# Optimization experiments

Measured on AMD Instinct MI355X. Metric: run time of the kernel, lower is better.

Reference implementation:

```python
import jax, jax.numpy as jnp
import numpy as np

EPS = 1e-06


def setup_inputs() -> dict:
    key = jax.random.key(0)
    k1, k2, k3 = jax.random.split(key, 3)
    B, H, S, D = 4, 16, 4096, 64
    query = jax.random.normal(k1, (B, H, S, D), dtype=jnp.float32)
    key_t = jax.random.normal(k2, (B, H, S, D), dtype=jnp.float32)
    value = jax.random.normal(k3, (B, H, S, D), dtype=jnp.float32)
    return {"query": query, "key": key_t, "value": value}


def _cosformer_features(x, cos_idx, sin_idx):
    # x: [B,H,S,D]; cos_idx/sin_idx: [S,1] -> features [B,H,S,2D]
    x_relu = jax.nn.relu(x)
    return jnp.concatenate([x_relu * cos_idx, x_relu * sin_idx], axis=-1)


def reference(query, key, value):
    B, H, S, D = query.shape
    query = query / jnp.sqrt(jnp.asarray(D, dtype=query.dtype))
    # idx = (pi/2) * [1..S]; angles divided by seq_len
    ang = (jnp.pi / 2) * jnp.arange(1, S + 1, dtype=query.dtype) / S  # [S]
    cos_idx = jnp.cos(ang)[:, None]  # [S,1]
    sin_idx = jnp.sin(ang)[:, None]  # [S,1]
    q_cs = _cosformer_features(query, cos_idx, sin_idx)  # [B,H,S,2D]
    k_cs = _cosformer_features(key, cos_idx, sin_idx)    # [B,H,S,2D]
    # norm: 1 / clamp(q_cs . sum_l(k_cs), eps)
    k_sum = jnp.sum(k_cs, axis=-2)  # [B,H,2D]
    norm = 1.0 / jnp.maximum(jnp.einsum('bhld,bhd->bhl', q_cs, k_sum), EPS)  # [B,H,S]
    # linear attention: KV aggregation then query projection
    kv = jnp.einsum('bhld,bhlm->bhdm', k_cs, value)  # [B,H,2D,D]
    out = jnp.einsum('bhld,bhdm->bhlm', q_cs, kv) * norm[..., None]  # [B,H,S,D]
    return out
```

## Files before the change

kernel.cpp:

```cpp
#include <hip/hip_runtime.h>
#include <hip/hip_bf16.h>
#include <math.h>
#include <stdint.h>

#define BHN    64
#define SEQ    4096
#define DIM    64
#define NCHUNK 8
#define CHUNK  (SEQ / NCHUNK)
#define KSTEP  32
#define NIT    (CHUNK / KSTEP)
#define KVF    (128 * DIM)
#define STRIDE_C ((size_t)BHN * KVF + (size_t)BHN * 128)
#define KSBASE ((size_t)BHN * KVF)
#define FRAGH  10240
#define LPADT  40

typedef __bf16 bf16x8v __attribute__((ext_vector_type(8)));
typedef float  f32x4v  __attribute__((ext_vector_type(4)));

__device__ inline f32x4v mfma16(bf16x8v a, bf16x8v b, f32x4v c) {
    return __builtin_amdgcn_mfma_f32_16x16x32_bf16(a, b, c, 0, 0, 0);
}

__device__ inline unsigned pk2(float a, float b) {
    __hip_bfloat162 t(__float2bfloat16(a), __float2bfloat16(b));
    return *(unsigned*)&t;
}

__device__ __forceinline__ void barrier_noflush() {
    asm volatile("s_waitcnt lgkmcnt(0)" ::: "memory");
    __builtin_amdgcn_s_barrier();
    asm volatile("" ::: "memory");
}

__device__ __forceinline__ void gload16(const float* g, const float* lds_base) {
    __builtin_amdgcn_global_load_lds(
        (const __attribute__((address_space(1))) void*)(uintptr_t)g,
        (__attribute__((address_space(3)))  void*)(uintptr_t)lds_base,
        16, 0, 0);
}

template<int USE_ATOMIC>
__global__ __launch_bounds__(512) void cosformer_kv_mfma(
    const float* __restrict__ K, const float* __restrict__ V,
    float* __restrict__ part)
{
    __shared__ float  rawK[3][KSTEP][DIM];
    __shared__ float  rawV[3][KSTEP][DIM];
    __shared__ ushort ktc[DIM][LPADT];
    __shared__ ushort kts[DIM][LPADT];
    __shared__ ushort vtt[DIM][LPADT];

    const int bh    = blockIdx.x / NCHUNK;
    const int chunk = blockIdx.x % NCHUNK;
    const int row0  = chunk * CHUNK;
    const float* Kb = K + (size_t)bh * SEQ * DIM;
    const float* Vb = V + (size_t)bh * SEQ * DIM;

    const int tid  = threadIdx.x;
    const int lane = tid & 63;
    const int w    = tid >> 6;
    const int g2    = (tid >> 4) & 15;
    const int dq    = (tid & 15) * 4;
    const int kvsel = tid >> 8;
    const int frow = lane & 15;
    const int kgrp = lane >> 4;
    const int d0   = (w & 3) * 16 + frow;

    f32x4v acc[5];
    #pragma unroll
    for (int t = 0; t < 5; ++t) acc[t] = (f32x4v){0.f, 0.f, 0.f, 0.f};

    bf16x8v onef;
    #pragma unroll
    for (int j = 0; j < 8; ++j) onef[j] = (frow == 0) ? (__bf16)1.0f : (__bf16)0.0f;

    auto STAGE = [&](int it) {
        const int buf = it % 3;
        const size_t go = (size_t)(row0 + it * KSTEP) * DIM + w * 256 + lane * 4;
        gload16(Kb + go, &rawK[buf][w * 4][0]);
        gload16(Vb + go, &rawV[buf][w * 4][0]);
    };

    auto TRANSFORM = [&](int it) {
        const int buf = it % 3;
        const int r = 2 * g2;
        if (kvsel == 0) {
            float4 k0 = *(const float4*)&rawK[buf][r][dq];
            float4 k1 = *(const float4*)&rawK[buf][r + 1][dq];
            const int l0 = row0 + it * KSTEP + r;
            const float CC = 1.5707963267948966f / (float)SEQ;
            float s0v, c0, s1v, c1;
            __sincosf(CC * (float)(l0 + 1), &s0v, &c0);
            __sincosf(CC * (float)(l0 + 2), &s1v, &c1);
            float a0[4] = {k0.x, k0.y, k0.z, k0.w};
            float a1[4] = {k1.x, k1.y, k1.z, k1.w};
            #pragma unroll
            for (int i = 0; i < 4; ++i) {
                const int d = dq + i;
                const int c = g2 ^ (4 * ((d >> 2) & 3));
                float r0 = fmaxf(a0[i], 0.f), r1 = fmaxf(a1[i], 0.f);
                ((unsigned*)&ktc[d][0])[c] = pk2(r0 * c0,  r1 * c1);
                ((unsigned*)&kts[d][0])[c] = pk2(r0 * s0v, r1 * s1v);
            }
        } else {
            float4 v0q = *(const float4*)&rawV[buf][r][dq];
            float4 v1q = *(const float4*)&rawV[buf][r + 1][dq];
            float a0[4] = {v0q.x, v0q.y, v0q.z, v0q.w};
            float a1[4] = {v1q.x, v1q.y, v1q.z, v1q.w};
            #pragma unroll
            for (int i = 0; i < 4; ++i) {
                const int d = dq + i;
                const int c = g2 ^ (4 * ((d >> 2) & 3));
                ((unsigned*)&vtt[d][0])[c] = pk2(a0[i], a1[i]);
            }
        }
    };

    STAGE(0);
    STAGE(1);

    #pragma unroll 1
    for (int it = 0; it < NIT; ++it) {
        if (it + 1 < NIT) asm volatile("s_waitcnt vmcnt(2)" ::: "memory");
        else              asm volatile("s_waitcnt vmcnt(0)" ::: "memory");
        __builtin_amdgcn_sched_barrier(0);
        barrier_noflush();

        if (it + 2 < NIT) STAGE(it + 2);

        TRANSFORM(it);
        barrier_noflush();

        const ushort (*ap)[LPADT] = (w < 4) ? ktc : kts;
        {
            const int ca = (kgrp * 4) ^ (4 * ((d0 >> 2) & 3));
            bf16x8v a = *(const bf16x8v*)&ap[d0][2 * ca];
            #pragma unroll
            for (int nt = 0; nt < 4; ++nt) {
                const int dn = nt * 16 + frow;
                const int cb = (kgrp * 4) ^ (4 * ((dn >> 2) & 3));
                bf16x8v b = *(const bf16x8v*)&vtt[dn][2 * cb];
                acc[nt] = mfma16(a, b, acc[nt]);
            }
            acc[4] = mfma16(a, onef, acc[4]);
        }
    }

    const int fb = w * 16 + kgrp * 4;
    if (USE_ATOMIC) {
        float* pb = part + (size_t)bh * KVF;
        float* ps = part + KSBASE + bh * 128;
        #pragma unroll
        for (int nt = 0; nt < 4; ++nt)
            #pragma unroll
            for (int r = 0; r < 4; ++r)
                atomicAdd(&pb[(size_t)(fb + r) * DIM + nt * 16 + frow], acc[nt][r]);
        if (frow == 0)
            #pragma unroll
            for (int r = 0; r < 4; ++r) atomicAdd(&ps[fb + r], acc[4][r]);
    } else {
        float* pb = part + STRIDE_C * chunk + (size_t)bh * KVF;
        float* ps = part + STRIDE_C * chunk + KSBASE + bh * 128;
        #pragma unroll
        for (int nt = 0; nt < 4; ++nt)
            #pragma unroll
            for (int r = 0; r < 4; ++r)
                pb[(size_t)(fb + r) * DIM + nt * 16 + frow] = acc[nt][r];
        if (frow == 0)
            #pragma unroll
            for (int r = 0; r < 4; ++r) ps[fb + r] = acc[4][r];
    }
}

template<int NC>
__global__ __launch_bounds__(256) void reduce_pack(
    const float* __restrict__ part, __hip_bfloat16* __restrict__ bfrag)
{
    size_t o = (size_t)blockIdx.x * 256 + threadIdx.x;
    float s = 0.f;
    #pragma unroll
    for (int c = 0; c < NC; ++c) s += part[(size_t)c * STRIDE_C + o];
    if (o < KSBASE) {
        int head = (int)(o >> 13);
        int r = (int)(o & 8191);
        int k = r >> 6, n = r & 63;
        int t = n >> 4, ks = k >> 5, lg = (k >> 3) & 3, j = k & 7;
        int lane = lg * 16 + (n & 15);
        bfrag[(size_t)head * FRAGH + (size_t)(((t * 4 + ks) * 64 + lane) * 8 + j)] =
            __float2bfloat16(s);
    } else {
        int r = (int)(o - KSBASE);
        int head = r >> 7, k = r & 127;
        int ks = k >> 5, lg = (k >> 3) & 3, j = k & 7;
        bfrag[(size_t)head * FRAGH + (size_t)(((16 + ks) * 64 + lg * 16) * 8 + j)] =
            __float2bfloat16(s);
    }
}

__global__ __launch_bounds__(256) void cosformer_out_mfma(
    const float* __restrict__ Q, const __hip_bfloat16* __restrict__ bfrag,
    float* __restrict__ out)
{
    __shared__ __hip_bfloat16 sb[FRAGH];
    const int head = blockIdx.x >> 3;
    const int tile = blockIdx.x & 7;
    const int tid  = threadIdx.x;

    {
        const float4* src = (const float4*)(bfrag + (size_t)head * FRAGH);
        float4* dst = (float4*)sb;
        #pragma unroll
        for (int i = 0; i < 5; ++i) dst[tid + 256 * i] = src[tid + 256 * i];
    }

    const int lane = tid & 63;
    const int w    = tid >> 6;
    const int mrow = lane & 15;
    const int kgrp = lane >> 4;

    const float* Qb = Q + (size_t)head * SEQ * DIM;
    float*       Ob = out + (size_t)head * SEQ * DIM;
    const int rowblk = tile * 512;

    float4 qb[2][4];
    #pragma unroll
    for (int m = 0; m < 2; ++m) {
        const float4* qr = (const float4*)(Qb + (size_t)(rowblk + w * 32 + m * 16 + mrow) * DIM);
        qb[m][0] = qr[kgrp * 2];
        qb[m][1] = qr[kgrp * 2 + 1];
        qb[m][2] = qr[8 + kgrp * 2];
        qb[m][3] = qr[8 + kgrp * 2 + 1];
    }

    barrier_noflush();

    #pragma unroll
    for (int g = 0; g < 4; ++g) {
        const int base = rowblk + (g * 4 + w) * 32;

        bf16x8v af[2][4];
        #pragma unroll
        for (int m = 0; m < 2; ++m) {
            int arow = base + m * 16 + mrow;
            float ang = 1.5707963267948966f * (float)(arow + 1) / (float)SEQ;
            float sn, cn;
            __sincosf(ang, &sn, &cn);
            float crs = cn * 0.125f, srs = sn * 0.125f;
            float lo[8] = {qb[m][0].x, qb[m][0].y, qb[m][0].z, qb[m][0].w,
                           qb[m][1].x, qb[m][1].y, qb[m][1].z, qb[m][1].w};
            float hi[8] = {qb[m][2].x, qb[m][2].y, qb[m][2].z, qb[m][2].w,
                           qb[m][3].x, qb[m][3].y, qb[m][3].z, qb[m][3].w};
            #pragma unroll
            for (int j = 0; j < 8; ++j) {
                float rl = fmaxf(lo[j], 0.f);
                float rh = fmaxf(hi[j], 0.f);
                af[m][0][j] = (__bf16)(rl * crs);
                af[m][1][j] = (__bf16)(rh * crs);
                af[m][2][j] = (__bf16)(rl * srs);
                af[m][3][j] = (__bf16)(rh * srs);
            }
        }

        if (g < 3) {
            #pragma unroll
            for (int m = 0; m < 2; ++m) {
                const float4* qr = (const float4*)(Qb + (size_t)(rowblk + ((g + 1) * 4 + w) * 32 + m * 16 + mrow) * DIM);
                qb[m][0] = qr[kgrp * 2];
                qb[m][1] = qr[kgrp * 2 + 1];
                qb[m][2] = qr[8 + kgrp * 2];
                qb[m][3] = qr[8 + kgrp * 2 + 1];
            }
        }

        f32x4v acc[2][5];
        #pragma unroll
        for (int m = 0; m < 2; ++m)
            #pragma unroll
            for (int t = 0; t < 5; ++t)
                acc[m][t] = (f32x4v){0.f, 0.f, 0.f, 0.f};

        #pragma unroll
        for (int t = 0; t < 5; ++t)
            #pragma unroll
            for (int ks = 0; ks < 4; ++ks) {
                bf16x8v bf = *(const bf16x8v*)&sb[(size_t)(((t * 4 + ks) * 64 + lane) * 8)];
                acc[0][t] = mfma16(af[0][ks], bf, acc[0][t]);
                acc[1][t] = mfma16(af[1][ks], bf, acc[1][t]);
            }

        #pragma unroll
        for (int m = 0; m < 2; ++m) {
            #pragma unroll
            for (int r = 0; r < 4; ++r) {
                float den = __shfl(acc[m][4][r], lane & 48, 64);
                float invd = 1.0f / fmaxf(den, 1e-6f);
                int row = base + m * 16 + kgrp * 4 + r;
                float* op = Ob + (size_t)row * DIM + mrow;
                op[0]  = acc[m][0][r] * invd;
                op[16] = acc[m][1][r] * invd;
                op[32] = acc[m][2][r] * invd;
                op[48] = acc[m][3][r] * invd;
            }
        }
    }
}

extern "C" void kernel_launch(void* const* d_in, const int* in_sizes, int n_in,
                              void* d_out, int out_size, void* d_ws, size_t ws_size,
                              hipStream_t stream) {
    const float* Q = (const float*)d_in[0];
    const float* K = (const float*)d_in[1];
    const float* V = (const float*)d_in[2];
    float* out = (float*)d_out;
    float* ws  = (float*)d_ws;

    const size_t frag_bytes = (size_t)FRAGH * BHN * sizeof(__hip_bfloat16);
    const size_t need_full  = (size_t)NCHUNK * STRIDE_C * sizeof(float) + frag_bytes;

    if (ws_size >= need_full) {
        float* part = ws;
        __hip_bfloat16* bfrag = (__hip_bfloat16*)(ws + (size_t)NCHUNK * STRIDE_C);
        hipMemsetAsync(bfrag, 0, frag_bytes, stream);
        hipLaunchKernelGGL((cosformer_kv_mfma<0>), dim3(BHN * NCHUNK), dim3(512), 0, stream,
                           K, V, part);
        hipLaunchKernelGGL((reduce_pack<NCHUNK>), dim3((int)(STRIDE_C / 256)), dim3(256), 0, stream,
                           part, bfrag);
        hipLaunchKernelGGL(cosformer_out_mfma, dim3(BHN * 8), dim3(256), 0, stream,
                           Q, bfrag, out);
    } else {
        float* part = ws;
        __hip_bfloat16* bfrag = (__hip_bfloat16*)(ws + STRIDE_C);
        hipMemsetAsync(part, 0, STRIDE_C * sizeof(float), stream);
        hipMemsetAsync(bfrag, 0, frag_bytes, stream);
        hipLaunchKernelGGL((cosformer_kv_mfma<1>), dim3(BHN * NCHUNK), dim3(512), 0, stream,
                           K, V, part);
        hipLaunchKernelGGL((reduce_pack<1>), dim3((int)(STRIDE_C / 256)), dim3(256), 0, stream,
                           part, bfrag);
        hipLaunchKernelGGL(cosformer_out_mfma, dim3(BHN * 8), dim3(256), 0, stream,
                           Q, bfrag, out);
    }
}
```

Before: 71.63 us.

## Issue all chunk loads upfront and double the sequence chunk count

Doubles the number of sequence chunks per batch-head, so each block covers 256 rows (8 iterations). The 3-buffer rolling prefetch is replaced by issuing every K/V load for the whole chunk at kernel start into LDS, with per-iteration vmcnt waits that count down. This aims to keep more memory requests in flight and give the GPU twice as many blocks. In exchange, LDS use grows to about 128KB per block, which may limit blocks per CU, and the partial-sum reduction or atomic traffic doubles.

```diff
diff --git a/kernel.cpp b/kernel.cpp
--- a/kernel.cpp
+++ b/kernel.cpp
@@ -6,7 +6,7 @@
 #define BHN    64
 #define SEQ    4096
 #define DIM    64
-#define NCHUNK 8
+#define NCHUNK 16
 #define CHUNK  (SEQ / NCHUNK)
 #define KSTEP  32
 #define NIT    (CHUNK / KSTEP)
@@ -46,8 +46,8 @@
     const float* __restrict__ K, const float* __restrict__ V,
     float* __restrict__ part)
 {
-    __shared__ float  rawK[3][KSTEP][DIM];
-    __shared__ float  rawV[3][KSTEP][DIM];
+    __shared__ float  rawK[NIT][KSTEP][DIM];
+    __shared__ float  rawV[NIT][KSTEP][DIM];
     __shared__ ushort ktc[DIM][LPADT];
     __shared__ ushort kts[DIM][LPADT];
     __shared__ ushort vtt[DIM][LPADT];
@@ -76,19 +76,18 @@
     #pragma unroll
     for (int j = 0; j < 8; ++j) onef[j] = (frow == 0) ? (__bf16)1.0f : (__bf16)0.0f;
 
-    auto STAGE = [&](int it) {
-        const int buf = it % 3;
-        const size_t go = (size_t)(row0 + it * KSTEP) * DIM + w * 256 + lane * 4;
-        gload16(Kb + go, &rawK[buf][w * 4][0]);
-        gload16(Vb + go, &rawV[buf][w * 4][0]);
-    };
+    #pragma unroll
+    for (int t = 0; t < NIT; ++t) {
+        const size_t go = (size_t)(row0 + t * KSTEP) * DIM + w * 256 + lane * 4;
+        gload16(Kb + go, &rawK[t][w * 4][0]);
+        gload16(Vb + go, &rawV[t][w * 4][0]);
+    }
 
     auto TRANSFORM = [&](int it) {
-        const int buf = it % 3;
         const int r = 2 * g2;
         if (kvsel == 0) {
-            float4 k0 = *(const float4*)&rawK[buf][r][dq];
-            float4 k1 = *(const float4*)&rawK[buf][r + 1][dq];
+            float4 k0 = *(const float4*)&rawK[it][r][dq];
+            float4 k1 = *(const float4*)&rawK[it][r + 1][dq];
             const int l0 = row0 + it * KSTEP + r;
             const float CC = 1.5707963267948966f / (float)SEQ;
             float s0v, c0, s1v, c1;
@@ -105,8 +104,8 @@
                 ((unsigned*)&kts[d][0])[c] = pk2(r0 * s0v, r1 * s1v);
             }
         } else {
-            float4 v0q = *(const float4*)&rawV[buf][r][dq];
-            float4 v1q = *(const float4*)&rawV[buf][r + 1][dq];
+            float4 v0q = *(const float4*)&rawV[it][r][dq];
+            float4 v1q = *(const float4*)&rawV[it][r + 1][dq];
             float a0[4] = {v0q.x, v0q.y, v0q.z, v0q.w};
             float a1[4] = {v1q.x, v1q.y, v1q.z, v1q.w};
             #pragma unroll
@@ -118,34 +117,35 @@
         }
     };
 
-    STAGE(0);
-    STAGE(1);
-
-    #pragma unroll 1
+    #pragma unroll
     for (int it = 0; it < NIT; ++it) {
-        if (it + 1 < NIT) asm volatile("s_waitcnt vmcnt(2)" ::: "memory");
-        else              asm volatile("s_waitcnt vmcnt(0)" ::: "memory");
+        switch (it) {
+            case 0: asm volatile("s_waitcnt vmcnt(14)" ::: "memory"); break;
+            case 1: asm volatile("s_waitcnt vmcnt(12)" ::: "memory"); break;
+            case 2: asm volatile("s_waitcnt vmcnt(10)" ::: "memory"); break;
+            case 3: asm volatile("s_waitcnt vmcnt(8)"  ::: "memory"); break;
+            case 4: asm volatile("s_waitcnt vmcnt(6)"  ::: "memory"); break;
+            case 5: asm volatile("s_waitcnt vmcnt(4)"  ::: "memory"); break;
+            case 6: asm volatile("s_waitcnt vmcnt(2)"  ::: "memory"); break;
+            default: asm volatile("s_waitcnt vmcnt(0)" ::: "memory"); break;
+        }
         __builtin_amdgcn_sched_barrier(0);
         barrier_noflush();
 
-        if (it + 2 < NIT) STAGE(it + 2);
-
         TRANSFORM(it);
         barrier_noflush();
 
         const ushort (*ap)[LPADT] = (w < 4) ? ktc : kts;
-        {
-            const int ca = (kgrp * 4) ^ (4 * ((d0 >> 2) & 3));
-            bf16x8v a = *(const bf16x8v*)&ap[d0][2 * ca];
-            #pragma unroll
-            for (int nt = 0; nt < 4; ++nt) {
-                const int dn = nt * 16 + frow;
-                const int cb = (kgrp * 4) ^ (4 * ((dn >> 2) & 3));
-                bf16x8v b = *(const bf16x8v*)&vtt[dn][2 * cb];
-                acc[nt] = mfma16(a, b, acc[nt]);
-            }
-            acc[4] = mfma16(a, onef, acc[4]);
-        }
+        const int ca = (kgrp * 4) ^ (4 * ((d0 >> 2) & 3));
+        bf16x8v a = *(const bf16x8v*)&ap[d0][2 * ca];
+        #pragma unroll
+        for (int nt = 0; nt < 4; ++nt) {
+            const int dn = nt * 16 + frow;
+            const int cb = (kgrp * 4) ^ (4 * ((dn >> 2) & 3));
+            bf16x8v b = *(const bf16x8v*)&vtt[dn][2 * cb];
+            acc[nt] = mfma16(a, b, acc[nt]);
+        }
+        acc[4] = mfma16(a, onef, acc[4]);
     }
 
     const int fb = w * 16 + kgrp * 4;
```

New measurement: 90.84 us. 26.8% more time.
